# Kernel tuning notes

Measured on AMD Instinct MI355X. Metric: run time of the kernel, lower is better.

The kernel has to match this reference:

```python
import jax, jax.numpy as jnp
import numpy as np

B, N, P, D, OUT = 32, 52, 1024, 512, 607
_DENSE = [6, 64, 128, 256, 512, D]   # dense PointNet encoder channel sizes
_SPARSE = [6, 32, 64, D]             # sparse (relation) PointNet encoder channel sizes
_OM = [D, 128, 256, OUT]             # object_mlp hidden sizes


def setup_inputs() -> dict:
    key = jax.random.key(0)
    ks = jax.random.split(key, 40)

    def w(k, shape):
        return jax.random.normal(ks[k], shape, jnp.float32) * (1.0 / float(np.sqrt(shape[0])))

    inp = {}
    inp["input"] = jax.random.normal(ks[0], (B, 1024, 6), jnp.float32)
    inp["objects"] = jax.random.normal(ks[1], (B, N, P, 6), jnp.float32)
    inp["objects_length"] = jax.random.randint(ks[2], (B,), 1, N + 1)
    k = 3
    for i in range(5):
        inp[f"de_W{i}"] = w(k, (_DENSE[i], _DENSE[i + 1])); k += 1
        inp[f"de_b{i}"] = jnp.zeros((_DENSE[i + 1],), jnp.float32)
    for i in range(3):
        inp[f"se_W{i}"] = w(k, (_SPARSE[i], _SPARSE[i + 1])); k += 1
        inp[f"se_b{i}"] = jnp.zeros((_SPARSE[i + 1],), jnp.float32)
    for i in range(3):
        inp[f"om_W{i}"] = w(k, (_OM[i], _OM[i + 1])); k += 1
        inp[f"om_b{i}"] = jnp.zeros((_OM[i + 1],), jnp.float32)
    inp["r1_W"] = w(k, (2 * D, D)); k += 1
    inp["r1_b"] = jnp.zeros((D,), jnp.float32)
    inp["r2_W"] = w(k, (D, D)); k += 1
    inp["r2_b"] = jnp.zeros((D,), jnp.float32)
    inp["m1_W"] = w(k, (D, D)); k += 1
    inp["m1_b"] = jnp.zeros((D,), jnp.float32)
    inp["m2_W"] = w(k, (D, D)); k += 1
    inp["m2_b"] = jnp.zeros((D,), jnp.float32)
    return inp


def reference(input, objects, objects_length,
              de_W0, de_b0, de_W1, de_b1, de_W2, de_b2, de_W3, de_b3, de_W4, de_b4,
              se_W0, se_b0, se_W1, se_b1, se_W2, se_b2,
              om_W0, om_b0, om_W1, om_b1, om_W2, om_b2,
              r1_W, r1_b, r2_W, r2_b, m1_W, m1_b, m2_W, m2_b):
    relu = jax.nn.relu
    # --- sparse PointNet encoder on location-masked clouds (xyz kept, rest zeroed) ---
    masked = jnp.concatenate([objects[..., :3], jnp.zeros_like(objects[..., 3:])], axis=-1)
    h = masked  # [B, N, P, 6]
    for W, b in ((se_W0, se_b0), (se_W1, se_b1), (se_W2, se_b2)):
        h = relu(h @ W + b)
    pn_obj = jnp.transpose(h.max(axis=2), (1, 0, 2))  # [N, B, D]

    # --- all (i, j) pairwise union features, vectorized (replaces the N^2 python loop) ---
    fi = jnp.broadcast_to(pn_obj[:, None], (N, N, B, D))
    fj = jnp.broadcast_to(pn_obj[None, :], (N, N, B, D))
    u = relu(jnp.concatenate([fi, fj], axis=-1))        # [N, N, B, 2D]
    rel = u @ r1_W + r1_b                               # relation_dense_layer
    rel = relu(rel) @ r2_W + r2_b                       # relation_dense_layer_2 -> [N, N, B, D]
    multi = relu(rel) @ m1_W + m1_b                     # multi_relation_dense_layer
    multi = relu(multi) @ m2_W + m2_b                   # multi_relation_dense_layer_2

    # --- dense PointNet encoder + object MLP ---
    h = objects  # [B, N, P, 6]
    for W, b in ((de_W0, de_b0), (de_W1, de_b1), (de_W2, de_b2), (de_W3, de_b3), (de_W4, de_b4)):
        h = relu(h @ W + b)
    obj = jnp.transpose(h.max(axis=2), (1, 0, 2))       # [N, B, D]
    obj = relu(obj @ om_W0 + om_b0)
    obj = relu(obj @ om_W1 + om_b1)
    obj = obj @ om_W2 + om_b2                           # [N, B, 607]

    return obj, rel, multi
```

## Files before the change

### kernel.cpp

```cpp
#include <hip/hip_runtime.h>
#include <stdint.h>

typedef __attribute__((ext_vector_type(8))) __bf16 bf16x8;
typedef __attribute__((ext_vector_type(4))) float f32x4;
typedef __attribute__((ext_vector_type(8))) short short8;

__device__ __forceinline__ unsigned short f2bf(float f) {
  unsigned int u = __float_as_uint(f);
  u += 0x7FFFu + ((u >> 16) & 1u);
  return (unsigned short)(u >> 16);
}
__device__ __forceinline__ float bf2f(unsigned short h) {
  return __uint_as_float((unsigned int)h << 16);
}
__device__ __forceinline__ void split2(float v, unsigned short& h, unsigned short& l) {
  h = f2bf(v);
  l = f2bf(v - bf2f(h));
}

template<int COUT>
__global__ __launch_bounds__(512, 2)
void gemmX(const unsigned short* __restrict__ A,
           const unsigned short* __restrict__ Wt,
           const float* __restrict__ bias,
           void* __restrict__ Cdst, void* __restrict__ Cdst2,
           unsigned int* __restrict__ Omax,
           int M, int K, int ldc, int ntn, int swz8, int m_base)
{
  extern __shared__ __align__(16) char smem[];
  short* Ab0 = (short*)smem;
  short* Bb0 = (short*)(smem + 32768);
  short* Ab1 = (short*)(smem + 65536);
  short* Bb1 = (short*)(smem + 98304);

  int bid = blockIdx.x;
  int mt, nt;
  if (swz8) {
    int xcd = bid & 7;
    int slot = bid >> 3;
    nt = slot % ntn;
    mt = (slot / ntn) * 8 + xcd;
  } else {
    mt = bid / ntn;
    nt = bid - mt * ntn;
  }
  const int m0 = mt * 256, n0 = nt * 256;
  const int tid = threadIdx.x;
  const int lane = tid & 63;
  const int w = tid >> 6;
  const int wm = w >> 2, wn = w & 3;
  const int l15 = lane & 15, l4 = lane >> 4;
  const int lr = lane >> 3;
  const int kswz = ((lane & 7) ^ lr) * 8;

  const unsigned short* a_s[4];
  const unsigned short* b_s[4];
  #pragma unroll
  for (int i = 0; i < 4; ++i) {
    int row = i * 64 + w * 8 + lr;
    a_s[i] = A + (size_t)(m0 + row) * K + kswz;
    b_s[i] = Wt + (size_t)(n0 + row) * K + kswz;
  }

  f32x4 acc[8][4];
  #pragma unroll
  for (int a = 0; a < 8; ++a)
    #pragma unroll
    for (int b = 0; b < 4; ++b)
      acc[a][b] = (f32x4){0.f, 0.f, 0.f, 0.f};

  auto STAGE = [&](int kt, short* Ad, short* Bd) {
    int koff = kt * 64;
    #pragma unroll
    for (int i = 0; i < 4; ++i) {
      int rows = i * 64 + w * 8;
      __builtin_amdgcn_global_load_lds(a_s[i] + koff, (void*)(Ad + rows * 64), 16, 0, 0);
      __builtin_amdgcn_global_load_lds(b_s[i] + koff, (void*)(Bd + rows * 64), 16, 0, 0);
    }
  };

  STAGE(0, Ab0, Bb0);
  __syncthreads();

  const int NT = K >> 6;
  for (int kt = 0; kt < NT; ++kt) {
    int cur = kt & 1;
    short* Ac = cur ? Ab1 : Ab0;
    short* Bc = cur ? Bb1 : Bb0;
    if (kt + 1 < NT) STAGE(kt + 1, cur ? Ab0 : Ab1, cur ? Bb0 : Bb1);
    #pragma unroll
    for (int ks = 0; ks < 2; ++ks) {
      bf16x8 bv[4];
      #pragma unroll
      for (int ni = 0; ni < 4; ++ni) {
        int R = wn * 64 + ni * 16 + l15;
        int ph = (ks * 4 + l4) ^ (R & 7);
        bv[ni] = *reinterpret_cast<const bf16x8*>(&Bc[R * 64 + ph * 8]);
      }
      #pragma unroll
      for (int mh = 0; mh < 2; ++mh) {
        bf16x8 av[4];
        #pragma unroll
        for (int m4 = 0; m4 < 4; ++m4) {
          int R = wm * 128 + (mh * 4 + m4) * 16 + l15;
          int ph = (ks * 4 + l4) ^ (R & 7);
          av[m4] = *reinterpret_cast<const bf16x8*>(&Ac[R * 64 + ph * 8]);
        }
        __builtin_amdgcn_s_setprio(1);
        #pragma unroll
        for (int m4 = 0; m4 < 4; ++m4)
          #pragma unroll
          for (int ni = 0; ni < 4; ++ni)
            acc[mh * 4 + m4][ni] =
                __builtin_amdgcn_mfma_f32_16x16x32_bf16(av[m4], bv[ni], acc[mh * 4 + m4][ni], 0, 0, 0);
        __builtin_amdgcn_s_setprio(0);
      }
    }
    __syncthreads();
  }

  if (COUT == 2) {
    int obj = (m_base + m0) >> 10;
    #pragma unroll
    for (int ni = 0; ni < 4; ++ni) {
      int n = n0 + wn * 64 + ni * 16 + l15;
      float v = acc[0][ni][0];
      #pragma unroll
      for (int mi = 0; mi < 8; ++mi)
        #pragma unroll
        for (int i = 0; i < 4; ++i)
          v = fmaxf(v, acc[mi][ni][i]);
      v = fmaxf(v + bias[n], 0.0f);
      v = fmaxf(v, __shfl_xor(v, 16));
      v = fmaxf(v, __shfl_xor(v, 32));
      if (l4 == 0)
        atomicMax(&Omax[(size_t)obj * 512 + n], __float_as_uint(v));
    }
    return;
  }
  if (COUT == 0 || COUT == 3) {
    float* Bf = (float*)smem;
    float* Cf = (float*)Cdst;
    #pragma unroll
    for (int h = 0; h < 2; ++h) {
      if (wm == h) {
        #pragma unroll
        for (int mi = 0; mi < 8; ++mi)
          #pragma unroll
          for (int i = 0; i < 4; ++i) {
            int row = mi * 16 + l4 * 4 + i;
            #pragma unroll
            for (int ni = 0; ni < 4; ++ni) {
              int col = wn * 64 + ni * 16 + l15;
              int sl = col >> 2;
              int ph = (sl & 56) | ((sl & 7) ^ (row & 7));
              Bf[row * 256 + ph * 4 + (col & 3)] = acc[mi][ni][i] + bias[n0 + col];
            }
          }
      }
      __syncthreads();
      #pragma unroll
      for (int s = 0; s < 16; ++s) {
        int p = s * 512 + tid;
        int row = p >> 6, sl = p & 63;
        int ph = (sl & 56) | ((sl & 7) ^ (row & 7));
        f32x4 v = *reinterpret_cast<const f32x4*>(&Bf[row * 256 + ph * 4]);
        *reinterpret_cast<f32x4*>(Cf + (size_t)(m0 + h * 128 + row) * ldc + n0 + sl * 4) = v;
      }
      __syncthreads();
    }
  }
  if (COUT == 1 || COUT == 3) {
    unsigned short* Bp = (unsigned short*)smem;
    unsigned short* Cp = (unsigned short*)(COUT == 3 ? Cdst2 : Cdst);
    #pragma unroll
    for (int mi = 0; mi < 8; ++mi)
      #pragma unroll
      for (int i = 0; i < 4; ++i) {
        int row = wm * 128 + mi * 16 + l4 * 4 + i;
        #pragma unroll
        for (int ni = 0; ni < 4; ++ni) {
          int col = wn * 64 + ni * 16 + l15;
          int sl = col >> 3;
          int ph = (sl & 24) | ((sl & 7) ^ (row & 7));
          Bp[row * 256 + ph * 8 + (col & 7)] = f2bf(fmaxf(acc[mi][ni][i] + bias[n0 + col], 0.f));
        }
      }
    __syncthreads();
    #pragma unroll
    for (int s = 0; s < 16; ++s) {
      int p = s * 512 + tid;
      int row = p >> 5, sl = p & 31;
      int ph = (sl & 24) | ((sl & 7) ^ (row & 7));
      short8 v = *reinterpret_cast<const short8*>(&Bp[row * 256 + ph * 8]);
      *reinterpret_cast<short8*>(Cp + (size_t)(m0 + row) * ldc + n0 + sl * 8) = v;
    }
  }
}

template<int COUT>
__global__ __launch_bounds__(256)
void gemm3(const unsigned short* __restrict__ A,
           const unsigned short* __restrict__ Wt,
           const float* __restrict__ bias,
           void* __restrict__ Cdst,
           unsigned int* __restrict__ Omax,
           int M, int K, int ldc, int ntn, int swz8, int m_base)
{
  __shared__ __align__(16) short SM[3][128][64];

  int bid = blockIdx.x;
  int mt, nt;
  if (swz8) {
    int xcd = bid & 7;
    int slot = bid >> 3;
    nt = slot % ntn;
    mt = (slot / ntn) * 8 + xcd;
  } else {
    mt = bid / ntn;
    nt = bid - mt * ntn;
  }
  const int m0 = mt * 128, n0 = nt * 128;
  const int tid = threadIdx.x;
  const int lane = tid & 63;
  const int wave = tid >> 6;
  const int wm = wave >> 1, wn = wave & 1;
  const int l15 = lane & 15, l4 = lane >> 4;

  const int rr = tid >> 3;
  const int sp = tid & 7;
  const int sl = sp ^ (rr & 7);
  const int slE = sl * 8;

  const unsigned short* a_p[4];
  const unsigned short* b_p[4];
  #pragma unroll
  for (int c = 0; c < 4; ++c) {
    int rt = c * 32 + rr;
    a_p[c] = A + (size_t)(m0 + rt) * K + slE;
    b_p[c] = Wt + (size_t)(n0 + rt) * 2 * K + slE;
  }

  f32x4 acc[4][4];
  #pragma unroll
  for (int a = 0; a < 4; ++a)
    #pragma unroll
    for (int b = 0; b < 4; ++b)
      acc[a][b] = (f32x4){0.f, 0.f, 0.f, 0.f};

  char* const smb = (char*)&SM[0][0][0];

  for (int k0 = 0; k0 < K; k0 += 64) {
    #pragma unroll
    for (int c = 0; c < 4; ++c) {
      char* lb = smb + c * 4096 + (tid & 192) * 16;
      __builtin_amdgcn_global_load_lds(a_p[c] + k0, (void*)lb, 16, 0, 0);
      __builtin_amdgcn_global_load_lds(b_p[c] + k0, (void*)(lb + 16384), 16, 0, 0);
      __builtin_amdgcn_global_load_lds(b_p[c] + K + k0, (void*)(lb + 32768), 16, 0, 0);
    }
    __syncthreads();
    #pragma unroll
    for (int kf = 0; kf < 2; ++kf) {
      bf16x8 av[4], bh[4], bl[4];
      #pragma unroll
      for (int mi = 0; mi < 4; ++mi) {
        int R = wm * 64 + mi * 16 + l15;
        int sph = (kf * 4 + l4) ^ (R & 7);
        av[mi] = *reinterpret_cast<const bf16x8*>(&SM[0][R][sph * 8]);
      }
      #pragma unroll
      for (int ni = 0; ni < 4; ++ni) {
        int R = wn * 64 + ni * 16 + l15;
        int sph = (kf * 4 + l4) ^ (R & 7);
        bh[ni] = *reinterpret_cast<const bf16x8*>(&SM[1][R][sph * 8]);
        bl[ni] = *reinterpret_cast<const bf16x8*>(&SM[2][R][sph * 8]);
      }
      #pragma unroll
      for (int mi = 0; mi < 4; ++mi)
        #pragma unroll
        for (int ni = 0; ni < 4; ++ni) {
          acc[mi][ni] = __builtin_amdgcn_mfma_f32_16x16x32_bf16(av[mi], bh[ni], acc[mi][ni], 0, 0, 0);
          acc[mi][ni] = __builtin_amdgcn_mfma_f32_16x16x32_bf16(av[mi], bl[ni], acc[mi][ni], 0, 0, 0);
        }
    }
    __syncthreads();
  }

  if (COUT == 2) {
    int obj = (m_base + m0) >> 10;
    #pragma unroll
    for (int ni = 0; ni < 4; ++ni) {
      int n = n0 + wn * 64 + ni * 16 + l15;
      float v = acc[0][ni][0];
      #pragma unroll
      for (int mi = 0; mi < 4; ++mi)
        #pragma unroll
        for (int i = 0; i < 4; ++i)
          v = fmaxf(v, acc[mi][ni][i]);
      v = fmaxf(v + bias[n], 0.0f);
      v = fmaxf(v, __shfl_xor(v, 16));
      v = fmaxf(v, __shfl_xor(v, 32));
      if (l4 == 0)
        atomicMax(&Omax[(size_t)obj * 512 + n], __float_as_uint(v));
    }
  } else {
    float* Bf = (float*)smb;
    float* Cf = (float*)Cdst;
    #pragma unroll
    for (int h = 0; h < 2; ++h) {
      if (wm == h) {
        #pragma unroll
        for (int mi = 0; mi < 4; ++mi)
          #pragma unroll
          for (int i = 0; i < 4; ++i) {
            int lr2 = mi * 16 + l4 * 4 + i;
            #pragma unroll
            for (int ni = 0; ni < 4; ++ni) {
              int col = wn * 64 + ni * 16 + l15;
              int off = lr2 * 128 + (((col >> 2) ^ (lr2 & 7)) << 2) + (col & 3);
              Bf[off] = acc[mi][ni][i] + bias[n0 + col];
            }
          }
      }
      __syncthreads();
      #pragma unroll
      for (int s = 0; s < 8; ++s) {
        int p = tid * 8 + s;
        int row = p >> 5, ls = p & 31;
        f32x4 v = *reinterpret_cast<const f32x4*>(&Bf[row * 128 + ((ls ^ (row & 7)) << 2)]);
        *reinterpret_cast<f32x4*>(Cf + (size_t)(m0 + h * 64 + row) * ldc + n0 + ls * 4) = v;
      }
      __syncthreads();
    }
  }
}

__global__ __launch_bounds__(256)
void points_kernel(const float* __restrict__ obj6,
                   const float* __restrict__ sW0, const float* __restrict__ sb0,
                   const float* __restrict__ sW1, const float* __restrict__ sb1,
                   const float* __restrict__ dW0, const float* __restrict__ db0,
                   const float* __restrict__ dW1, const float* __restrict__ db1,
                   unsigned short* __restrict__ s2,
                   unsigned short* __restrict__ h2)
{
  __shared__ float sw0[96], sbb0[32], sw1[2048], sbb1[64];
  __shared__ float dw0[384], dbb0[64], dw1[8192], dbb1[128];
  int tid = threadIdx.x;
  for (int i = tid; i < 96; i += 256) sw0[i] = sW0[i];
  if (tid < 32) sbb0[tid] = sb0[tid];
  for (int i = tid; i < 2048; i += 256) sw1[i] = sW1[i];
  if (tid < 64) sbb1[tid] = sb1[tid];
  for (int i = tid; i < 384; i += 256) dw0[i] = dW0[i];
  if (tid < 64) dbb0[tid] = db0[tid];
  for (int i = tid; i < 8192; i += 256) dw1[i] = dW1[i];
  if (tid < 128) dbb1[tid] = db1[tid];
  __syncthreads();

  int pt = blockIdx.x * 256 + tid;
  const float* in = obj6 + (size_t)pt * 6;
  float c0 = in[0], c1 = in[1], c2 = in[2], c3 = in[3], c4 = in[4], c5 = in[5];

  {
    float h1[32];
    #pragma unroll
    for (int j = 0; j < 32; ++j)
      h1[j] = fmaxf(c0 * sw0[j] + c1 * sw0[32 + j] + c2 * sw0[64 + j] + sbb0[j], 0.f);
    unsigned short* orow = s2 + (size_t)pt * 64;
    #pragma unroll
    for (int j8 = 0; j8 < 8; ++j8) {
      float a[8];
      #pragma unroll
      for (int e = 0; e < 8; ++e) a[e] = sbb1[j8 * 8 + e];
      #pragma unroll
      for (int i = 0; i < 32; ++i) {
        float hv = h1[i];
        #pragma unroll
        for (int e = 0; e < 8; ++e) a[e] += hv * sw1[i * 64 + j8 * 8 + e];
      }
      short8 o;
      #pragma unroll
      for (int e = 0; e < 8; ++e) o[e] = (short)f2bf(fmaxf(a[e], 0.f));
      *reinterpret_cast<short8*>(orow + j8 * 8) = o;
    }
  }

  {
    float h1[64];
    #pragma unroll
    for (int j = 0; j < 64; ++j) {
      float a = dbb0[j] + c0 * dw0[j] + c1 * dw0[64 + j] + c2 * dw0[128 + j]
              + c3 * dw0[192 + j] + c4 * dw0[256 + j] + c5 * dw0[320 + j];
      h1[j] = fmaxf(a, 0.f);
    }
    unsigned short* orow = h2 + (size_t)pt * 128;
    #pragma unroll
    for (int ch = 0; ch < 4; ++ch) {
      float a[32];
      #pragma unroll
      for (int e = 0; e < 32; ++e) a[e] = dbb1[ch * 32 + e];
      #pragma unroll 8
      for (int i = 0; i < 64; ++i) {
        float hv = h1[i];
        #pragma unroll
        for (int e = 0; e < 32; ++e) a[e] += hv * dw1[i * 128 + ch * 32 + e];
      }
      #pragma unroll
      for (int e8 = 0; e8 < 4; ++e8) {
        short8 o;
        #pragma unroll
        for (int e = 0; e < 8; ++e) o[e] = (short)f2bf(fmaxf(a[e8 * 8 + e], 0.f));
        *reinterpret_cast<short8*>(orow + ch * 32 + e8 * 8) = o;
      }
    }
  }
}

__global__ void transpose_split(const float* __restrict__ W, unsigned short* __restrict__ Wt,
                                int K, int N)
{
  int id = blockIdx.x * 256 + threadIdx.x;
  if (id >= K * N) return;
  int k = id / N, n = id - k * N;
  unsigned short h, l;
  split2(W[id], h, l);
  Wt[(size_t)n * 2 * K + k] = h;
  Wt[(size_t)n * 2 * K + K + k] = l;
}

__global__ void transpose_cast(const float* __restrict__ W, unsigned short* __restrict__ Wt,
                               int K, int N)
{
  int id = blockIdx.x * 256 + threadIdx.x;
  if (id >= K * N) return;
  int k = id / N, n = id - k * N;
  Wt[(size_t)n * K + k] = f2bf(W[id]);
}

__global__ void zero_kernel(unsigned int* __restrict__ p, int n)
{
  int id = blockIdx.x * 256 + threadIdx.x;
  if (id < n) p[id] = 0u;
}

__global__ void pn_pack_kernel(const float* __restrict__ pnf, unsigned short* __restrict__ pnp)
{
  int id = blockIdx.x * 256 + threadIdx.x;
  int o = id >> 9, c = id & 511;
  int b = o / 52, n = o - b * 52;
  pnp[((size_t)(n * 32 + b) << 9) + c] = f2bf(pnf[id]);
}

__global__ __launch_bounds__(256)
void rel_combine_kernel(const float* __restrict__ G,
                        const float* __restrict__ bias, unsigned short* __restrict__ t1)
{
  int t = blockIdx.x * 256 + threadIdx.x;
  int r = t >> 6, c8 = (t & 63) << 3;
  int b = r & 31;
  int pair = r >> 5;
  int i = pair / 52;
  int j = pair - i * 52;
  const float* g1 = G + ((size_t)(i * 32 + b) << 10) + c8;
  const float* g2 = G + ((size_t)(j * 32 + b) << 10) + 512 + c8;
  short8 o;
  #pragma unroll
  for (int e = 0; e < 8; ++e)
    o[e] = (short)f2bf(fmaxf(g1[e] + g2[e] + bias[c8 + e], 0.f));
  *reinterpret_cast<short8*>(t1 + (size_t)r * 512 + c8) = o;
}

__global__ __launch_bounds__(256)
void objmlp_kernel(const float* __restrict__ obj,
                   const float* __restrict__ W0, const float* __restrict__ b0,
                   const float* __restrict__ W1, const float* __restrict__ b1,
                   const float* __restrict__ W2, const float* __restrict__ b2,
                   float* __restrict__ out)
{
  __shared__ float x[512];
  __shared__ float h1[128];
  __shared__ float h2[256];
  int tid = threadIdx.x;
  int r = blockIdx.x;
  int n = r >> 5, b = r & 31;
  int o = b * 52 + n;
  const float* xs = obj + (size_t)o * 512;
  x[tid] = xs[tid];
  x[tid + 256] = xs[tid + 256];
  __syncthreads();
  if (tid < 128) {
    float a = b0[tid];
    #pragma unroll 8
    for (int k = 0; k < 512; ++k) a += x[k] * W0[k * 128 + tid];
    h1[tid] = fmaxf(a, 0.f);
  }
  __syncthreads();
  {
    float a = b1[tid];
    #pragma unroll 8
    for (int k = 0; k < 128; ++k) a += h1[k] * W1[k * 256 + tid];
    h2[tid] = fmaxf(a, 0.f);
  }
  __syncthreads();
  for (int j = tid; j < 607; j += 256) {
    float a = b2[j];
    #pragma unroll 8
    for (int k = 0; k < 256; ++k) a += h2[k] * W2[k * 607 + j];
    out[(size_t)r * 607 + j] = a;
  }
}

extern "C" void kernel_launch(void* const* d_in, const int* in_sizes, int n_in,
                              void* d_out, int out_size, void* d_ws, size_t ws_size,
                              hipStream_t stream)
{
  const float* objects = (const float*)d_in[1];
  const float* de_W0 = (const float*)d_in[3];  const float* de_b0 = (const float*)d_in[4];
  const float* de_W1 = (const float*)d_in[5];  const float* de_b1 = (const float*)d_in[6];
  const float* de_W2 = (const float*)d_in[7];  const float* de_b2 = (const float*)d_in[8];
  const float* de_W3 = (const float*)d_in[9];  const float* de_b3 = (const float*)d_in[10];
  const float* de_W4 = (const float*)d_in[11]; const float* de_b4 = (const float*)d_in[12];
  const float* se_W0 = (const float*)d_in[13]; const float* se_b0 = (const float*)d_in[14];
  const float* se_W1 = (const float*)d_in[15]; const float* se_b1 = (const float*)d_in[16];
  const float* se_W2 = (const float*)d_in[17]; const float* se_b2 = (const float*)d_in[18];
  const float* om_W0 = (const float*)d_in[19]; const float* om_b0 = (const float*)d_in[20];
  const float* om_W1 = (const float*)d_in[21]; const float* om_b1 = (const float*)d_in[22];
  const float* om_W2 = (const float*)d_in[23]; const float* om_b2 = (const float*)d_in[24];
  const float* r1_W = (const float*)d_in[25];  const float* r1_b = (const float*)d_in[26];
  const float* r2_W = (const float*)d_in[27];  const float* r2_b = (const float*)d_in[28];
  const float* m1_W = (const float*)d_in[29];  const float* m1_b = (const float*)d_in[30];
  const float* m2_W = (const float*)d_in[31];  const float* m2_b = (const float*)d_in[32];
  (void)in_sizes; (void)n_in; (void)out_size;

  (void)hipFuncSetAttribute(reinterpret_cast<const void*>(&gemmX<0>),
                            hipFuncAttributeMaxDynamicSharedMemorySize, 131072);
  (void)hipFuncSetAttribute(reinterpret_cast<const void*>(&gemmX<1>),
                            hipFuncAttributeMaxDynamicSharedMemorySize, 131072);
  (void)hipFuncSetAttribute(reinterpret_cast<const void*>(&gemmX<2>),
                            hipFuncAttributeMaxDynamicSharedMemorySize, 131072);
  (void)hipFuncSetAttribute(reinterpret_cast<const void*>(&gemmX<3>),
                            hipFuncAttributeMaxDynamicSharedMemorySize, 131072);

  float* outf = (float*)d_out;
  float* out_obj = outf;
  float* out_rel = outf + 1010048;
  float* out_multi = out_rel + 44302336;

  char* ws = (char*)d_ws;
  size_t off = 0;
  auto alloc = [&](size_t bytes) -> void* {
    void* p = ws + off;
    off += (bytes + 255) & ~(size_t)255;
    return p;
  };
  unsigned short* wt_se2 = (unsigned short*)alloc((size_t)512 * 128 * 2);
  unsigned short* wt_de2 = (unsigned short*)alloc((size_t)256 * 128 * 2);
  unsigned short* wt_de3 = (unsigned short*)alloc((size_t)512 * 256 * 2);
  unsigned short* wt_de4 = (unsigned short*)alloc((size_t)512 * 512 * 2);
  unsigned short* wt_g   = (unsigned short*)alloc((size_t)1024 * 1024 * 2);
  unsigned short* wt_r2  = (unsigned short*)alloc((size_t)512 * 512 * 2);
  unsigned short* wt_m1  = (unsigned short*)alloc((size_t)512 * 512 * 2);
  unsigned short* wt_m2  = (unsigned short*)alloc((size_t)512 * 512 * 2);
  float* Gbuf = (float*)alloc((size_t)1664 * 1024 * 4);
  size_t avail = (ws_size > off + 256) ? (ws_size - off - 256) : 0;
  int Tc = (int)(avail / 262144);
  if (Tc < 1) Tc = 1;
  if (Tc > 338) Tc = 338;
  unsigned short* t2 = (unsigned short*)alloc((size_t)Tc * 262144);

  char* arena = (char*)out_rel;
  unsigned int* pnmax   = (unsigned int*)(arena);
  float*        obj_f32 = (float*)(arena + 3407872);
  unsigned short* pn_p  = (unsigned short*)(arena + 6815744);
  char* cbuf = arena + 8519680;
  const size_t PC = 131072;
  unsigned short* s2_c = (unsigned short*)(cbuf);
  unsigned short* h2_c = (unsigned short*)(cbuf + PC * 128);
  unsigned short* h3_c = (unsigned short*)(cbuf + PC * 384);
  unsigned short* h4_c = (unsigned short*)(cbuf + PC * 896);
  unsigned short* t1  = (unsigned short*)out_multi;
  unsigned short* t1b = (unsigned short*)((char*)out_multi + 88604672);

  zero_kernel<<<(2 * 851968) / 256, 256, 0, stream>>>(pnmax, 2 * 851968);

  auto tsplit = [&](const float* W, unsigned short* Dst, int K, int N) {
    int n = K * N;
    transpose_split<<<(n + 255) / 256, 256, 0, stream>>>(W, Dst, K, N);
  };
  auto tcast = [&](const float* W, unsigned short* Dst, int K, int N) {
    int n = K * N;
    transpose_cast<<<(n + 255) / 256, 256, 0, stream>>>(W, Dst, K, N);
  };
  tsplit(se_W2, wt_se2, 64, 512);
  tcast(de_W2, wt_de2, 128, 256);
  tcast(de_W3, wt_de3, 256, 512);
  tcast(de_W4, wt_de4, 512, 512);
  tsplit(r1_W,             wt_g,              512, 512);
  tsplit(r1_W + 512 * 512, wt_g + 512 * 1024, 512, 512);
  tcast(r2_W,  wt_r2, 512, 512);
  tcast(m1_W,  wt_m1, 512, 512);
  tcast(m2_W,  wt_m2, 512, 512);

  for (int c = 0; c < 13; ++c) {
    int base = c * (int)PC;
    points_kernel<<<PC / 256, 256, 0, stream>>>(
        objects + (size_t)base * 6,
        se_W0, se_b0, se_W1, se_b1, de_W0, de_b0, de_W1, de_b1, s2_c, h2_c);
    gemm3<2><<<4 * (PC / 128), 256, 0, stream>>>(
        s2_c, wt_se2, se_b2, nullptr, pnmax, PC, 64, 512, 4, 1, base);
    gemmX<1><<<1 * (PC / 256), 512, 131072, stream>>>(
        h2_c, wt_de2, de_b2, h3_c, nullptr, nullptr, PC, 128, 256, 1, 1, 0);
    gemmX<1><<<2 * (PC / 256), 512, 131072, stream>>>(
        h3_c, wt_de3, de_b3, h4_c, nullptr, nullptr, PC, 256, 512, 2, 1, 0);
    gemmX<2><<<2 * (PC / 256), 512, 131072, stream>>>(
        h4_c, wt_de4, de_b4, nullptr, nullptr, (unsigned int*)obj_f32, PC, 512, 512, 2, 1, base);
  }

  pn_pack_kernel<<<851968 / 256, 256, 0, stream>>>((const float*)pnmax, pn_p);
  objmlp_kernel<<<1664, 256, 0, stream>>>(obj_f32, om_W0, om_b0, om_W1, om_b1,
                                          om_W2, om_b2, out_obj);

  zero_kernel<<<4, 256, 0, stream>>>((unsigned int*)t2, 1024);
  gemm3<0><<<13 * 8, 256, 0, stream>>>(
      pn_p, wt_g, (const float*)t2, Gbuf, nullptr, 1664, 512, 1024, 8, 0, 0);
  rel_combine_kernel<<<86528 * 64 / 256, 256, 0, stream>>>(Gbuf, r1_b, t1);
  gemmX<3><<<338 * 2, 512, 131072, stream>>>(
      t1, wt_r2, r2_b, out_rel, t1b, nullptr, 86528, 512, 512, 2, 0, 0);
  for (int tb = 0; tb < 338; tb += Tc) {
    int tiles = (338 - tb < Tc) ? (338 - tb) : Tc;
    int rows = tiles * 256;
    size_t rb = (size_t)tb * 256 * 512;
    gemmX<1><<<tiles * 2, 512, 131072, stream>>>(
        t1b + rb, wt_m1, m1_b, t2, nullptr, nullptr, rows, 512, 512, 2, 0, 0);
    gemmX<0><<<tiles * 2, 512, 131072, stream>>>(
        t2, wt_m2, m2_b, out_multi + rb, nullptr, nullptr, rows, 512, 512, 2, 0, 0);
  }
}
```

Before: 3.933 ms.

## Deepen gemmX pipeline to 4-stage K=32 ring with compile-time K and vmcnt waits

Rewrites the gemmX main loop to use a 4-slot shared-memory ring of K=32 tiles, prefetching three stages ahead and waiting with explicit vmcnt counts plus a raw barrier instead of a full __syncthreads per iteration. K becomes a template parameter so the loop fully unrolls. The sparse-encoder layer 3 GEMM moves from the split-bf16 gemm3 path (hi+lo weights, 2x MFMAs) to single-bf16 gemmX, which lowers precision for that layer. Launch bounds drop to one block per CU, which trades occupancy for deeper prefetch.

```diff
diff --git a/kernel.cpp b/kernel.cpp
--- a/kernel.cpp
+++ b/kernel.cpp
@@ -18,20 +18,20 @@
   l = f2bf(v - bf2f(h));
 }
 
-template<int COUT>
-__global__ __launch_bounds__(512, 2)
+#define WAITVM0 asm volatile("s_waitcnt vmcnt(0)" ::: "memory")
+#define WAITVM4 asm volatile("s_waitcnt vmcnt(4)" ::: "memory")
+#define WAITVM8 asm volatile("s_waitcnt vmcnt(8)" ::: "memory")
+
+template<int COUT, int K>
+__global__ __launch_bounds__(512, 1)
 void gemmX(const unsigned short* __restrict__ A,
            const unsigned short* __restrict__ Wt,
            const float* __restrict__ bias,
            void* __restrict__ Cdst, void* __restrict__ Cdst2,
            unsigned int* __restrict__ Omax,
-           int M, int K, int ldc, int ntn, int swz8, int m_base)
+           int M, int ldc, int ntn, int swz8, int m_base)
 {
   extern __shared__ __align__(16) char smem[];
-  short* Ab0 = (short*)smem;
-  short* Bb0 = (short*)(smem + 32768);
-  short* Ab1 = (short*)(smem + 65536);
-  short* Bb1 = (short*)(smem + 98304);
 
   int bid = blockIdx.x;
   int mt, nt;
@@ -50,16 +50,15 @@
   const int w = tid >> 6;
   const int wm = w >> 2, wn = w & 3;
   const int l15 = lane & 15, l4 = lane >> 4;
-  const int lr = lane >> 3;
-  const int kswz = ((lane & 7) ^ lr) * 8;
-
-  const unsigned short* a_s[4];
-  const unsigned short* b_s[4];
+
+  const unsigned short* aSrc[2];
+  const unsigned short* bSrc[2];
   #pragma unroll
-  for (int i = 0; i < 4; ++i) {
-    int row = i * 64 + w * 8 + lr;
-    a_s[i] = A + (size_t)(m0 + row) * K + kswz;
-    b_s[i] = Wt + (size_t)(n0 + row) * K + kswz;
+  for (int o = 0; o < 2; ++o) {
+    int ar = w * 32 + o * 16 + (lane >> 2);
+    int sc = ((lane & 3) ^ ((ar >> 1) & 3)) * 8;
+    aSrc[o] = A + (size_t)(m0 + ar) * K + sc;
+    bSrc[o] = Wt + (size_t)(n0 + ar) * K + sc;
   }
 
   f32x4 acc[8][4];
@@ -69,55 +68,63 @@
     for (int b = 0; b < 4; ++b)
       acc[a][b] = (f32x4){0.f, 0.f, 0.f, 0.f};
 
-  auto STAGE = [&](int kt, short* Ad, short* Bd) {
-    int koff = kt * 64;
-    #pragma unroll
-    for (int i = 0; i < 4; ++i) {
-      int rows = i * 64 + w * 8;
-      __builtin_amdgcn_global_load_lds(a_s[i] + koff, (void*)(Ad + rows * 64), 16, 0, 0);
-      __builtin_amdgcn_global_load_lds(b_s[i] + koff, (void*)(Bd + rows * 64), 16, 0, 0);
+  constexpr int NT = K / 32;
+
+  auto STAGE = [&](int kt) {
+    short* Ab = (short*)(smem + (size_t)(kt & 3) * 32768);
+    short* Bb = Ab + 8192;
+    int koff = kt * 32;
+    #pragma unroll
+    for (int o = 0; o < 2; ++o) {
+      int rows = w * 32 + o * 16;
+      __builtin_amdgcn_global_load_lds(aSrc[o] + koff, (void*)(Ab + rows * 32), 16, 0, 0);
+      __builtin_amdgcn_global_load_lds(bSrc[o] + koff, (void*)(Bb + rows * 32), 16, 0, 0);
     }
   };
 
-  STAGE(0, Ab0, Bb0);
+  STAGE(0);
+  if (NT > 1) STAGE(1);
+  if (NT > 2) STAGE(2);
+
+  #pragma unroll
+  for (int kt = 0; kt < NT; ++kt) {
+    const int beyond = (NT - 1 - kt < 2) ? (NT - 1 - kt) : 2;
+    if (beyond == 0)      { WAITVM0; }
+    else if (beyond == 1) { WAITVM4; }
+    else                  { WAITVM8; }
+    __builtin_amdgcn_sched_barrier(0);
+    __builtin_amdgcn_s_barrier();
+    __builtin_amdgcn_sched_barrier(0);
+
+    short* Ab = (short*)(smem + (size_t)(kt & 3) * 32768);
+    short* Bb = Ab + 8192;
+
+    bf16x8 aF[8], bF[4];
+    #pragma unroll
+    for (int n = 0; n < 4; ++n) {
+      int R = wn * 64 + n * 16 + l15;
+      int ph = l4 ^ ((R >> 1) & 3);
+      bF[n] = *reinterpret_cast<const bf16x8*>(Bb + R * 32 + ph * 8);
+    }
+    #pragma unroll
+    for (int m = 0; m < 8; ++m) {
+      int R = wm * 128 + m * 16 + l15;
+      int ph = l4 ^ ((R >> 1) & 3);
+      aF[m] = *reinterpret_cast<const bf16x8*>(Ab + R * 32 + ph * 8);
+    }
+
+    if (kt + 3 <= NT - 1) STAGE(kt + 3);
+
+    __builtin_amdgcn_s_setprio(1);
+    #pragma unroll
+    for (int m = 0; m < 8; ++m)
+      #pragma unroll
+      for (int n = 0; n < 4; ++n)
+        acc[m][n] = __builtin_amdgcn_mfma_f32_16x16x32_bf16(aF[m], bF[n], acc[m][n], 0, 0, 0);
+    __builtin_amdgcn_s_setprio(0);
+  }
+
   __syncthreads();
-
-  const int NT = K >> 6;
-  for (int kt = 0; kt < NT; ++kt) {
-    int cur = kt & 1;
-    short* Ac = cur ? Ab1 : Ab0;
-    short* Bc = cur ? Bb1 : Bb0;
-    if (kt + 1 < NT) STAGE(kt + 1, cur ? Ab0 : Ab1, cur ? Bb0 : Bb1);
-    #pragma unroll
-    for (int ks = 0; ks < 2; ++ks) {
-      bf16x8 bv[4];
-      #pragma unroll
-      for (int ni = 0; ni < 4; ++ni) {
-        int R = wn * 64 + ni * 16 + l15;
-        int ph = (ks * 4 + l4) ^ (R & 7);
-        bv[ni] = *reinterpret_cast<const bf16x8*>(&Bc[R * 64 + ph * 8]);
-      }
-      #pragma unroll
-      for (int mh = 0; mh < 2; ++mh) {
-        bf16x8 av[4];
-        #pragma unroll
-        for (int m4 = 0; m4 < 4; ++m4) {
-          int R = wm * 128 + (mh * 4 + m4) * 16 + l15;
-          int ph = (ks * 4 + l4) ^ (R & 7);
-          av[m4] = *reinterpret_cast<const bf16x8*>(&Ac[R * 64 + ph * 8]);
-        }
-        __builtin_amdgcn_s_setprio(1);
-        #pragma unroll
-        for (int m4 = 0; m4 < 4; ++m4)
-          #pragma unroll
-          for (int ni = 0; ni < 4; ++ni)
-            acc[mh * 4 + m4][ni] =
-                __builtin_amdgcn_mfma_f32_16x16x32_bf16(av[m4], bv[ni], acc[mh * 4 + m4][ni], 0, 0, 0);
-        __builtin_amdgcn_s_setprio(0);
-      }
-    }
-    __syncthreads();
-  }
 
   if (COUT == 2) {
     int obj = (m_base + m0) >> 10;
@@ -198,28 +205,17 @@
   }
 }
 
-template<int COUT>
 __global__ __launch_bounds__(256)
 void gemm3(const unsigned short* __restrict__ A,
            const unsigned short* __restrict__ Wt,
            const float* __restrict__ bias,
            void* __restrict__ Cdst,
-           unsigned int* __restrict__ Omax,
-           int M, int K, int ldc, int ntn, int swz8, int m_base)
+           int M, int K, int ldc, int ntn)
 {
   __shared__ __align__(16) short SM[3][128][64];
 
   int bid = blockIdx.x;
-  int mt, nt;
-  if (swz8) {
-    int xcd = bid & 7;
-    int slot = bid >> 3;
-    nt = slot % ntn;
-    mt = (slot / ntn) * 8 + xcd;
-  } else {
-    mt = bid / ntn;
-    nt = bid - mt * ntn;
-  }
+  int mt = bid / ntn, nt = bid - mt * ntn;
   const int m0 = mt * 128, n0 = nt * 128;
   const int tid = threadIdx.x;
   const int lane = tid & 63;
@@ -286,52 +282,33 @@
     __syncthreads();
   }
 
-  if (COUT == 2) {
-    int obj = (m_base + m0) >> 10;
-    #pragma unroll
-    for (int ni = 0; ni < 4; ++ni) {
-      int n = n0 + wn * 64 + ni * 16 + l15;
-      float v = acc[0][ni][0];
+  float* Bf = (float*)smb;
+  float* Cf = (float*)Cdst;
+  #pragma unroll
+  for (int h = 0; h < 2; ++h) {
+    if (wm == h) {
       #pragma unroll
       for (int mi = 0; mi < 4; ++mi)
         #pragma unroll
-        for (int i = 0; i < 4; ++i)
-          v = fmaxf(v, acc[mi][ni][i]);
-      v = fmaxf(v + bias[n], 0.0f);
-      v = fmaxf(v, __shfl_xor(v, 16));
-      v = fmaxf(v, __shfl_xor(v, 32));
-      if (l4 == 0)
-        atomicMax(&Omax[(size_t)obj * 512 + n], __float_as_uint(v));
-    }
-  } else {
-    float* Bf = (float*)smb;
-    float* Cf = (float*)Cdst;
-    #pragma unroll
-    for (int h = 0; h < 2; ++h) {
-      if (wm == h) {
-        #pragma unroll
-        for (int mi = 0; mi < 4; ++mi)
+        for (int i = 0; i < 4; ++i) {
+          int lr2 = mi * 16 + l4 * 4 + i;
           #pragma unroll
-          for (int i = 0; i < 4; ++i) {
-            int lr2 = mi * 16 + l4 * 4 + i;
-            #pragma unroll
-            for (int ni = 0; ni < 4; ++ni) {
-              int col = wn * 64 + ni * 16 + l15;
-              int off = lr2 * 128 + (((col >> 2) ^ (lr2 & 7)) << 2) + (col & 3);
-              Bf[off] = acc[mi][ni][i] + bias[n0 + col];
-            }
+          for (int ni = 0; ni < 4; ++ni) {
+            int col = wn * 64 + ni * 16 + l15;
+            int off = lr2 * 128 + (((col >> 2) ^ (lr2 & 7)) << 2) + (col & 3);
+            Bf[off] = acc[mi][ni][i] + bias[n0 + col];
           }
-      }
-      __syncthreads();
-      #pragma unroll
-      for (int s = 0; s < 8; ++s) {
-        int p = tid * 8 + s;
-        int row = p >> 5, ls = p & 31;
-        f32x4 v = *reinterpret_cast<const f32x4*>(&Bf[row * 128 + ((ls ^ (row & 7)) << 2)]);
-        *reinterpret_cast<f32x4*>(Cf + (size_t)(m0 + h * 64 + row) * ldc + n0 + ls * 4) = v;
-      }
-      __syncthreads();
-    }
+        }
+    }
+    __syncthreads();
+    #pragma unroll
+    for (int s = 0; s < 8; ++s) {
+      int p = tid * 8 + s;
+      int row = p >> 5, ls = p & 31;
+      f32x4 v = *reinterpret_cast<const f32x4*>(&Bf[row * 128 + ((ls ^ (row & 7)) << 2)]);
+      *reinterpret_cast<f32x4*>(Cf + (size_t)(m0 + h * 64 + row) * ldc + n0 + ls * 4) = v;
+    }
+    __syncthreads();
   }
 }
 
@@ -532,13 +509,19 @@
   const float* m2_W = (const float*)d_in[31];  const float* m2_b = (const float*)d_in[32];
   (void)in_sizes; (void)n_in; (void)out_size;
 
-  (void)hipFuncSetAttribute(reinterpret_cast<const void*>(&gemmX<0>),
+  (void)hipFuncSetAttribute(reinterpret_cast<const void*>(&gemmX<1, 128>),
                             hipFuncAttributeMaxDynamicSharedMemorySize, 131072);
-  (void)hipFuncSetAttribute(reinterpret_cast<const void*>(&gemmX<1>),
+  (void)hipFuncSetAttribute(reinterpret_cast<const void*>(&gemmX<1, 256>),
                             hipFuncAttributeMaxDynamicSharedMemorySize, 131072);
-  (void)hipFuncSetAttribute(reinterpret_cast<const void*>(&gemmX<2>),
+  (void)hipFuncSetAttribute(reinterpret_cast<const void*>(&gemmX<2, 512>),
                             hipFuncAttributeMaxDynamicSharedMemorySize, 131072);
-  (void)hipFuncSetAttribute(reinterpret_cast<const void*>(&gemmX<3>),
+  (void)hipFuncSetAttribute(reinterpret_cast<const void*>(&gemmX<2, 64>),
+                            hipFuncAttributeMaxDynamicSharedMemorySize, 131072);
+  (void)hipFuncSetAttribute(reinterpret_cast<const void*>(&gemmX<3, 512>),
+                            hipFuncAttributeMaxDynamicSharedMemorySize, 131072);
+  (void)hipFuncSetAttribute(reinterpret_cast<const void*>(&gemmX<1, 512>),
+                            hipFuncAttributeMaxDynamicSharedMemorySize, 131072);
+  (void)hipFuncSetAttribute(reinterpret_cast<const void*>(&gemmX<0, 512>),
                             hipFuncAttributeMaxDynamicSharedMemorySize, 131072);
 
   float* outf = (float*)d_out;
@@ -553,7 +536,7 @@
     off += (bytes + 255) & ~(size_t)255;
     return p;
   };
-  unsigned short* wt_se2 = (unsigned short*)alloc((size_t)512 * 128 * 2);
+  unsigned short* wt_se2 = (unsigned short*)alloc((size_t)512 * 64 * 2);
   unsigned short* wt_de2 = (unsigned short*)alloc((size_t)256 * 128 * 2);
   unsigned short* wt_de3 = (unsigned short*)alloc((size_t)512 * 256 * 2);
   unsigned short* wt_de4 = (unsigned short*)alloc((size_t)512 * 512 * 2);
@@ -591,7 +574,7 @@
     int n = K * N;
     transpose_cast<<<(n + 255) / 256, 256, 0, stream>>>(W, Dst, K, N);
   };
-  tsplit(se_W2, wt_se2, 64, 512);
+  tcast(se_W2, wt_se2, 64, 512);
   tcast(de_W2, wt_de2, 128, 256);
   tcast(de_W3, wt_de3, 256, 512);
   tcast(de_W4, wt_de4, 512, 512);
@@ -606,14 +589,14 @@
     points_kernel<<<PC / 256, 256, 0, stream>>>(
         objects + (size_t)base * 6,
         se_W0, se_b0, se_W1, se_b1, de_W0, de_b0, de_W1, de_b1, s2_c, h2_c);
-    gemm3<2><<<4 * (PC / 128), 256, 0, stream>>>(
-        s2_c, wt_se2, se_b2, nullptr, pnmax, PC, 64, 512, 4, 1, base);
-    gemmX<1><<<1 * (PC / 256), 512, 131072, stream>>>(
-        h2_c, wt_de2, de_b2, h3_c, nullptr, nullptr, PC, 128, 256, 1, 1, 0);
-    gemmX<1><<<2 * (PC / 256), 512, 131072, stream>>>(
-        h3_c, wt_de3, de_b3, h4_c, nullptr, nullptr, PC, 256, 512, 2, 1, 0);
-    gemmX<2><<<2 * (PC / 256), 512, 131072, stream>>>(
-        h4_c, wt_de4, de_b4, nullptr, nullptr, (unsigned int*)obj_f32, PC, 512, 512, 2, 1, base);
+    gemmX<2, 64><<<2 * (PC / 256), 512, 131072, stream>>>(
+        s2_c, wt_se2, se_b2, nullptr, nullptr, pnmax, PC, 512, 2, 1, base);
+    gemmX<1, 128><<<1 * (PC / 256), 512, 131072, stream>>>(
+        h2_c, wt_de2, de_b2, h3_c, nullptr, nullptr, PC, 256, 1, 1, 0);
+    gemmX<1, 256><<<2 * (PC / 256), 512, 131072, stream>>>(
+        h3_c, wt_de3, de_b3, h4_c, nullptr, nullptr, PC, 512, 2, 1, 0);
+    gemmX<2, 512><<<2 * (PC / 256), 512, 131072, stream>>>(
+        h4_c, wt_de4, de_b4, nullptr, nullptr, (unsigned int*)obj_f32, PC, 512, 2, 1, base);
   }
 
   pn_pack_kernel<<<851968 / 256, 256, 0, stream>>>((const float*)pnmax, pn_p);
@@ -621,18 +604,18 @@
                                           om_W2, om_b2, out_obj);
 
   zero_kernel<<<4, 256, 0, stream>>>((unsigned int*)t2, 1024);
-  gemm3<0><<<13 * 8, 256, 0, stream>>>(
-      pn_p, wt_g, (const float*)t2, Gbuf, nullptr, 1664, 512, 1024, 8, 0, 0);
+  gemm3<<<13 * 8, 256, 0, stream>>>(
+      pn_p, wt_g, (const float*)t2, Gbuf, 1664, 512, 1024, 8);
   rel_combine_kernel<<<86528 * 64 / 256, 256, 0, stream>>>(Gbuf, r1_b, t1);
-  gemmX<3><<<338 * 2, 512, 131072, stream>>>(
-      t1, wt_r2, r2_b, out_rel, t1b, nullptr, 86528, 512, 512, 2, 0, 0);
+  gemmX<3, 512><<<338 * 2, 512, 131072, stream>>>(
+      t1, wt_r2, r2_b, out_rel, t1b, nullptr, 86528, 512, 2, 0, 0);
   for (int tb = 0; tb < 338; tb += Tc) {
     int tiles = (338 - tb < Tc) ? (338 - tb) : Tc;
     int rows = tiles * 256;
     size_t rb = (size_t)tb * 256 * 512;
-    gemmX<1><<<tiles * 2, 512, 131072, stream>>>(
-        t1b + rb, wt_m1, m1_b, t2, nullptr, nullptr, rows, 512, 512, 2, 0, 0);
-    gemmX<0><<<tiles * 2, 512, 131072, stream>>>(
-        t2, wt_m2, m2_b, out_multi + rb, nullptr, nullptr, rows, 512, 512, 2, 0, 0);
-  }
-}
+    gemmX<1, 512><<<tiles * 2, 512, 131072, stream>>>(
+        t1b + rb, wt_m1, m1_b, t2, nullptr, nullptr, rows, 512, 2, 0, 0);
+    gemmX<0, 512><<<tiles * 2, 512, 131072, stream>>>(
+        t2, wt_m2, m2_b, out_multi + rb, nullptr, nullptr, rows, 512, 2, 0, 0);
+  }
+}
```

New measurement: 3.881 ms. Within noise of the previous version (-1.3%).
